# Kernel optimization log

Hardware: AMD Instinct MI355X
Metric: run time of the kernel (lower is better)

Reference implementation:

```python
import jax, jax.numpy as jnp
import numpy as np

D_IN, D_MODEL = 512, 256
B, N = 2, 512


def setup_inputs() -> dict:
    key = jax.random.key(0)
    ks = jax.random.split(key, 8)
    xav_x = float(np.sqrt(2.0 / (D_IN + D_MODEL)))
    xav_p = float(np.sqrt(2.0 / (4 + D_MODEL)))
    return {
        "x": jax.random.normal(ks[0], (B, N, D_IN), dtype=jnp.float32),
        "pos": jax.random.normal(ks[1], (B, N, 4), dtype=jnp.float32),
        "attn_mask": jax.random.randint(ks[2], (B, N, N), 0, 2, dtype=jnp.int32),
        "Wx": jax.random.normal(ks[3], (D_IN, D_MODEL), dtype=jnp.float32) * xav_x,
        "bx": jnp.zeros((D_MODEL,), dtype=jnp.float32),
        "Wp": jax.random.normal(ks[4], (4, D_MODEL), dtype=jnp.float32) * xav_p,
        "bp": jnp.zeros((D_MODEL,), dtype=jnp.float32),
        "w": jax.random.normal(ks[5], (D_MODEL,), dtype=jnp.float32) * 0.05,
    }


def reference(x, pos, attn_mask, Wx, bx, Wp, bp, w):
    # projected, activated inputs: [B, N, d_model]
    h = jnp.tanh(x @ Wx + bx)
    # pairwise relative positions: [B, N, N, 4]
    rel = pos[:, :, None, :] - pos[:, None, :, :]
    # position MLP + tanh: [B, N, N, d_model]
    z = jnp.tanh(rel @ Wp + bp)
    # scores via dot with weight vector: [B, N, N]
    attn = jnp.einsum("bijd,d->bij", z, w)
    mask = attn_mask != 0
    attn = jnp.where(mask, attn, -jnp.inf)
    attn = jax.nn.softmax(attn, axis=2)
    attn = jnp.where(mask, attn, 0.0)
    # dropout is identity in eval mode
    # weighted sum: [B, N, d_model]
    output = jnp.einsum("bij,bjd->bid", attn, h)
    return (output, attn)
```

## Files before the change

kernel.cpp:

```cpp
#include <hip/hip_runtime.h>
#include <hip/hip_bf16.h>
#include <math.h>

#define BATCH   2
#define SEQ     512
#define DIN     512
#define DM      256

#define LOG2E2  2.88539008177792681f

#if __has_builtin(__builtin_amdgcn_exp2f)
#define EXP2(x) __builtin_amdgcn_exp2f(x)
#else
#define EXP2(x) exp2f(x)
#endif
#if __has_builtin(__builtin_amdgcn_rcpf)
#define RCP(x) __builtin_amdgcn_rcpf(x)
#else
#define RCP(x) (1.0f / (x))
#endif

__device__ __forceinline__ float tanh_from_scaled(float targ) {
    return fmaf(-2.0f, RCP(1.0f + EXP2(targ)), 1.0f);
}

__global__ __launch_bounds__(512) void pre_k(
    const float* __restrict__ pos,
    const float* __restrict__ Wp,
    const float* __restrict__ bp,
    float* __restrict__ EA,
    float4* __restrict__ EB4)
{
    const int tid = threadIdx.x;

    if (blockIdx.x < 128) {
        const int b  = blockIdx.x >> 6;
        const int q  = blockIdx.x & 63;
        const int d0 = 4 * q;
        const float4 p = ((const float4*)pos)[b * SEQ + tid];
        float e[4];
        #pragma unroll
        for (int i = 0; i < 4; i++) {
            const int d = d0 + i;
            const float P = fmaf(p.x, Wp[d], fmaf(p.y, Wp[DM + d],
                            fmaf(p.z, Wp[2*DM + d], p.w * Wp[3*DM + d])));
            e[i] = EXP2(-LOG2E2 * P);
        }
        EB4[((size_t)(b * 64 + q)) * SEQ + tid] = make_float4(e[0], e[1], e[2], e[3]);
        return;
    }

    const int idx = blockIdx.x - 128;
    const int r2  = __builtin_amdgcn_readfirstlane(tid >> 8);
    const int d   = tid & 255;
    const int row = idx * 2 + r2;
    const float4 p = ((const float4*)pos)[row];
    const float P = fmaf(p.x, Wp[d],
                    fmaf(p.y, Wp[DM + d],
                    fmaf(p.z, Wp[2*DM + d],
                         p.w * Wp[3*DM + d])));
    EA[(size_t)row * DM + d] = EXP2(LOG2E2 * (P + bp[d]));
}

__global__ __launch_bounds__(256) void h_k(
    const float* __restrict__ x,
    const float* __restrict__ Wx,
    const float* __restrict__ bx,
    float* __restrict__ h)
{
    __shared__ float s_xt[32][68];
    __shared__ float s_wt[64][32];

    const int tid = threadIdx.x;
    const int rt  = blockIdx.x >> 3;
    const int ct  = blockIdx.x & 7;
    const int tx  = tid & 7;
    const int ty  = tid >> 3;

    float4 acc = make_float4(0.f, 0.f, 0.f, 0.f);

    for (int ks = 0; ks < 8; ks++) {
        const int k0 = ks * 64;
        #pragma unroll
        for (int s = 0; s < 2; s++) {
            const int fidx = tid * 2 + s;
            const int r = fidx >> 4, c = fidx & 15;
            const float4 v = *(const float4*)(x + (size_t)(rt * 32 + r) * DIN + k0 + 4 * c);
            *(float4*)&s_xt[r][4 * c] = v;
        }
        #pragma unroll
        for (int s = 0; s < 2; s++) {
            const int fidx = tid * 2 + s;
            const int r = fidx >> 3, c = fidx & 7;
            *(float4*)&s_wt[r][4 * c] =
                *(const float4*)(Wx + (size_t)(k0 + r) * DM + ct * 32 + 4 * c);
        }
        __syncthreads();

        #pragma unroll 8
        for (int k = 0; k < 64; k++) {
            const float  xv = s_xt[ty][k];
            const float4 wq = *(const float4*)&s_wt[k][4 * tx];
            acc.x = fmaf(xv, wq.x, acc.x);
            acc.y = fmaf(xv, wq.y, acc.y);
            acc.z = fmaf(xv, wq.z, acc.z);
            acc.w = fmaf(xv, wq.w, acc.w);
        }
        __syncthreads();
    }

    const float4 bq = *(const float4*)(bx + ct * 32 + 4 * tx);
    float4 t;
    t.x = tanh_from_scaled(LOG2E2 * (acc.x + bq.x));
    t.y = tanh_from_scaled(LOG2E2 * (acc.y + bq.y));
    t.z = tanh_from_scaled(LOG2E2 * (acc.z + bq.z));
    t.w = tanh_from_scaled(LOG2E2 * (acc.w + bq.w));
    *(float4*)(h + (size_t)(rt * 32 + ty) * DM + ct * 32 + 4 * tx) = t;
}

__global__ __launch_bounds__(512) void score_k(
    const int*   __restrict__ mask,
    const float* __restrict__ wv,
    const float* __restrict__ EA,
    const float4* __restrict__ EB4,
    float* __restrict__ attn_out)
{
    const int b   = blockIdx.x >> 8;
    const int i0  = (blockIdx.x & 255) * 2;
    const int tid = threadIdx.x;
    const int l   = tid & 63;

    __shared__ float4 s_eaA[64], s_eaB[64];
    __shared__ float  s_red[2][8];

    if (tid < 64) {
        s_eaA[tid] = *(const float4*)(EA + (size_t)(b * SEQ + i0) * DM + 4 * tid);
    } else if (tid < 128) {
        s_eaB[tid - 64] = *(const float4*)(EA + (size_t)(b * SEQ + i0 + 1) * DM + 4 * (tid - 64));
    }
    __syncthreads();

    const float4* __restrict__ EBj = EB4 + (size_t)b * 64 * SEQ + tid;

    float aA = 0.f, aB = 0.f;
    #pragma unroll 8
    for (int q = 0; q < 64; q++) {
        const float4 eb = EBj[(size_t)q * SEQ];
        const float4 eA = s_eaA[q];
        const float4 eB = s_eaB[q];
        const float4 wq = *(const float4*)(wv + 4 * q);

        const float yA0 = fmaf(eA.x, eb.x, 1.0f);
        const float yA1 = fmaf(eA.y, eb.y, 1.0f);
        const float yA2 = fmaf(eA.z, eb.z, 1.0f);
        const float yA3 = fmaf(eA.w, eb.w, 1.0f);
        aA = fmaf(fmaf(wq.y, yA0, wq.x * yA1), RCP(yA0 * yA1), aA);
        aA = fmaf(fmaf(wq.w, yA2, wq.z * yA3), RCP(yA2 * yA3), aA);

        const float yB0 = fmaf(eB.x, eb.x, 1.0f);
        const float yB1 = fmaf(eB.y, eb.y, 1.0f);
        const float yB2 = fmaf(eB.z, eb.z, 1.0f);
        const float yB3 = fmaf(eB.w, eb.w, 1.0f);
        aB = fmaf(fmaf(wq.y, yB0, wq.x * yB1), RCP(yB0 * yB1), aB);
        aB = fmaf(fmaf(wq.w, yB2, wq.z * yB3), RCP(yB2 * yB3), aB);
    }

    const size_t mrowA = (size_t)b * SEQ * SEQ + (size_t)i0 * SEQ + tid;
    const int mA = mask[mrowA];
    const int mB = mask[mrowA + SEQ];
    float pA = mA ? EXP2(-LOG2E2 * aA) : 0.f;
    float pB = mB ? EXP2(-LOG2E2 * aB) : 0.f;

    float sA = pA, sB = pB;
    #pragma unroll
    for (int off = 32; off; off >>= 1) {
        sA += __shfl_xor(sA, off, 64);
        sB += __shfl_xor(sB, off, 64);
    }
    const int w = tid >> 6;
    if (l == 0) { s_red[0][w] = sA; s_red[1][w] = sB; }
    __syncthreads();

    const float4 ra = ((const float4*)s_red[0])[0], rb = ((const float4*)s_red[0])[1];
    const float4 rc = ((const float4*)s_red[1])[0], rd = ((const float4*)s_red[1])[1];
    pA *= __fdividef(1.0f, (ra.x+ra.y+ra.z+ra.w) + (rb.x+rb.y+rb.z+rb.w));
    pB *= __fdividef(1.0f, (rc.x+rc.y+rc.z+rc.w) + (rd.x+rd.y+rd.z+rd.w));

    attn_out[mrowA]       = pA;
    attn_out[mrowA + SEQ] = pB;
}

__global__ __launch_bounds__(512) void av_k(
    const float* __restrict__ attn_out,
    const float* __restrict__ h,
    float* __restrict__ out)
{
    const int b   = blockIdx.x >> 7;
    const int i0  = (blockIdx.x & 127) * 4;
    const int tid = threadIdx.x;
    const int dq  = tid & 63;
    const int js  = __builtin_amdgcn_readfirstlane(tid >> 6);

    __shared__ float s_av[7][4][DM];

    const float* __restrict__ hp = h + (size_t)(b * SEQ + js * 64) * DM + 4 * dq;
    const float* __restrict__ ar0 = attn_out + (size_t)b * SEQ * SEQ
                                  + (size_t)i0 * SEQ + js * 64;
    const float* __restrict__ ar1 = ar0 + SEQ;
    const float* __restrict__ ar2 = ar0 + 2 * SEQ;
    const float* __restrict__ ar3 = ar0 + 3 * SEQ;

    float4 a0 = make_float4(0,0,0,0), a1 = a0, a2 = a0, a3 = a0;
    #pragma unroll 4
    for (int jj = 0; jj < 16; jj++) {
        const float4 P0 = *(const float4*)(ar0 + 4 * jj);
        const float4 P1 = *(const float4*)(ar1 + 4 * jj);
        const float4 P2 = *(const float4*)(ar2 + 4 * jj);
        const float4 P3 = *(const float4*)(ar3 + 4 * jj);
        const float4 h0 = *(const float4*)(hp + (size_t)(4*jj + 0) * DM);
        const float4 h1 = *(const float4*)(hp + (size_t)(4*jj + 1) * DM);
        const float4 h2 = *(const float4*)(hp + (size_t)(4*jj + 2) * DM);
        const float4 h3 = *(const float4*)(hp + (size_t)(4*jj + 3) * DM);

        a0.x = fmaf(P0.x,h0.x,fmaf(P0.y,h1.x,fmaf(P0.z,h2.x,fmaf(P0.w,h3.x,a0.x))));
        a0.y = fmaf(P0.x,h0.y,fmaf(P0.y,h1.y,fmaf(P0.z,h2.y,fmaf(P0.w,h3.y,a0.y))));
        a0.z = fmaf(P0.x,h0.z,fmaf(P0.y,h1.z,fmaf(P0.z,h2.z,fmaf(P0.w,h3.z,a0.z))));
        a0.w = fmaf(P0.x,h0.w,fmaf(P0.y,h1.w,fmaf(P0.z,h2.w,fmaf(P0.w,h3.w,a0.w))));
        a1.x = fmaf(P1.x,h0.x,fmaf(P1.y,h1.x,fmaf(P1.z,h2.x,fmaf(P1.w,h3.x,a1.x))));
        a1.y = fmaf(P1.x,h0.y,fmaf(P1.y,h1.y,fmaf(P1.z,h2.y,fmaf(P1.w,h3.y,a1.y))));
        a1.z = fmaf(P1.x,h0.z,fmaf(P1.y,h1.z,fmaf(P1.z,h2.z,fmaf(P1.w,h3.z,a1.z))));
        a1.w = fmaf(P1.x,h0.w,fmaf(P1.y,h1.w,fmaf(P1.z,h2.w,fmaf(P1.w,h3.w,a1.w))));
        a2.x = fmaf(P2.x,h0.x,fmaf(P2.y,h1.x,fmaf(P2.z,h2.x,fmaf(P2.w,h3.x,a2.x))));
        a2.y = fmaf(P2.x,h0.y,fmaf(P2.y,h1.y,fmaf(P2.z,h2.y,fmaf(P2.w,h3.y,a2.y))));
        a2.z = fmaf(P2.x,h0.z,fmaf(P2.y,h1.z,fmaf(P2.z,h2.z,fmaf(P2.w,h3.z,a2.z))));
        a2.w = fmaf(P2.x,h0.w,fmaf(P2.y,h1.w,fmaf(P2.z,h2.w,fmaf(P2.w,h3.w,a2.w))));
        a3.x = fmaf(P3.x,h0.x,fmaf(P3.y,h1.x,fmaf(P3.z,h2.x,fmaf(P3.w,h3.x,a3.x))));
        a3.y = fmaf(P3.x,h0.y,fmaf(P3.y,h1.y,fmaf(P3.z,h2.y,fmaf(P3.w,h3.y,a3.y))));
        a3.z = fmaf(P3.x,h0.z,fmaf(P3.y,h1.z,fmaf(P3.z,h2.z,fmaf(P3.w,h3.z,a3.z))));
        a3.w = fmaf(P3.x,h0.w,fmaf(P3.y,h1.w,fmaf(P3.z,h2.w,fmaf(P3.w,h3.w,a3.w))));
    }

    if (js > 0) {
        *(float4*)&s_av[js - 1][0][4 * dq] = a0;
        *(float4*)&s_av[js - 1][1][4 * dq] = a1;
        *(float4*)&s_av[js - 1][2][4 * dq] = a2;
        *(float4*)&s_av[js - 1][3][4 * dq] = a3;
    }
    __syncthreads();
    if (js == 0) {
        #pragma unroll
        for (int s = 0; s < 7; s++) {
            const float4 q0 = *(const float4*)&s_av[s][0][4 * dq];
            const float4 q1 = *(const float4*)&s_av[s][1][4 * dq];
            const float4 q2 = *(const float4*)&s_av[s][2][4 * dq];
            const float4 q3 = *(const float4*)&s_av[s][3][4 * dq];
            a0.x += q0.x; a0.y += q0.y; a0.z += q0.z; a0.w += q0.w;
            a1.x += q1.x; a1.y += q1.y; a1.z += q1.z; a1.w += q1.w;
            a2.x += q2.x; a2.y += q2.y; a2.z += q2.z; a2.w += q2.w;
            a3.x += q3.x; a3.y += q3.y; a3.z += q3.z; a3.w += q3.w;
        }
        float* __restrict__ op = out + (size_t)(b * SEQ + i0) * DM + 4 * dq;
        *(float4*)(op)          = a0;
        *(float4*)(op + DM)     = a1;
        *(float4*)(op + 2*DM)   = a2;
        *(float4*)(op + 3*DM)   = a3;
    }
}

extern "C" void kernel_launch(void* const* d_in, const int* in_sizes, int n_in,
                              void* d_out, int out_size, void* d_ws, size_t ws_size,
                              hipStream_t stream) {
    const float* x    = (const float*)d_in[0];
    const float* pos  = (const float*)d_in[1];
    const int*   mask = (const int*)  d_in[2];
    const float* Wx   = (const float*)d_in[3];
    const float* bx   = (const float*)d_in[4];
    const float* Wp   = (const float*)d_in[5];
    const float* bp   = (const float*)d_in[6];
    const float* wv   = (const float*)d_in[7];

    float* out      = (float*)d_out;
    float* attn_out = (float*)d_out + (size_t)BATCH*SEQ*DM;

    char*   ws  = (char*)d_ws;
    float*  h   = (float*)(ws);
    float*  EA  = (float*)(ws + (size_t)BATCH*SEQ*DM*4);
    float4* EB4 = (float4*)(ws + 2*(size_t)BATCH*SEQ*DM*4);

    pre_k  <<<128 + (BATCH*SEQ)/2, 512, 0, stream>>>(pos, Wp, bp, EA, EB4);
    h_k    <<<256, 256, 0, stream>>>(x, Wx, bx, h);
    score_k<<<(BATCH*SEQ)/2, 512, 0, stream>>>(mask, wv, EA, EB4, attn_out);
    av_k   <<<(BATCH*SEQ)/4, 512, 0, stream>>>(attn_out, h, out);
}
```

Measured before the change: 114.5 us.

## Fuse four kernels into two: merge producers and fuse score with AV

Merges the EA/EB precompute and the x@Wx+tanh projection into one producer kernel, and fuses the softmax-score kernel with the attention-times-h reduction so probabilities stay in shared memory instead of being re-read from global. The number of launches drops from four to two. The h projection now reads Wx directly from global memory instead of staging it in LDS, and each attend block redoes the h reads for only two rows instead of four, which raises total h traffic.

```diff
diff --git a/kernel.cpp b/kernel.cpp
--- a/kernel.cpp
+++ b/kernel.cpp
@@ -24,12 +24,16 @@
     return fmaf(-2.0f, RCP(1.0f + EXP2(targ)), 1.0f);
 }
 
-__global__ __launch_bounds__(512) void pre_k(
+__global__ __launch_bounds__(512) void produce_k(
     const float* __restrict__ pos,
     const float* __restrict__ Wp,
     const float* __restrict__ bp,
+    const float* __restrict__ x,
+    const float* __restrict__ Wx,
+    const float* __restrict__ bx,
     float* __restrict__ EA,
-    float4* __restrict__ EB4)
+    float4* __restrict__ EB4,
+    float* __restrict__ h)
 {
     const int tid = threadIdx.x;
 
@@ -50,57 +54,44 @@
         return;
     }
 
-    const int idx = blockIdx.x - 128;
-    const int r2  = __builtin_amdgcn_readfirstlane(tid >> 8);
-    const int d   = tid & 255;
-    const int row = idx * 2 + r2;
-    const float4 p = ((const float4*)pos)[row];
-    const float P = fmaf(p.x, Wp[d],
-                    fmaf(p.y, Wp[DM + d],
-                    fmaf(p.z, Wp[2*DM + d],
-                         p.w * Wp[3*DM + d])));
-    EA[(size_t)row * DM + d] = EXP2(LOG2E2 * (P + bp[d]));
-}
-
-__global__ __launch_bounds__(256) void h_k(
-    const float* __restrict__ x,
-    const float* __restrict__ Wx,
-    const float* __restrict__ bx,
-    float* __restrict__ h)
-{
     __shared__ float s_xt[32][68];
-    __shared__ float s_wt[64][32];
-
-    const int tid = threadIdx.x;
-    const int rt  = blockIdx.x >> 3;
-    const int ct  = blockIdx.x & 7;
-    const int tx  = tid & 7;
-    const int ty  = tid >> 3;
+
+    const int idx  = blockIdx.x - 128;
+    const int rt   = idx >> 2;
+    const int ct   = idx & 3;
+    const int ty   = tid >> 4;
+    const int tx   = tid & 15;
+    const int row  = rt * 32 + ty;
+    const int dcol = ct * 64 + 4 * tx;
+
+    {
+        const float4 p  = ((const float4*)pos)[row];
+        const float4 w0 = *(const float4*)(Wp + dcol);
+        const float4 w1 = *(const float4*)(Wp + DM + dcol);
+        const float4 w2 = *(const float4*)(Wp + 2*DM + dcol);
+        const float4 w3 = *(const float4*)(Wp + 3*DM + dcol);
+        const float4 bq = *(const float4*)(bp + dcol);
+        float4 ea;
+        ea.x = EXP2(LOG2E2 * (fmaf(p.x,w0.x,fmaf(p.y,w1.x,fmaf(p.z,w2.x,p.w*w3.x))) + bq.x));
+        ea.y = EXP2(LOG2E2 * (fmaf(p.x,w0.y,fmaf(p.y,w1.y,fmaf(p.z,w2.y,p.w*w3.y))) + bq.y));
+        ea.z = EXP2(LOG2E2 * (fmaf(p.x,w0.z,fmaf(p.y,w1.z,fmaf(p.z,w2.z,p.w*w3.z))) + bq.z));
+        ea.w = EXP2(LOG2E2 * (fmaf(p.x,w0.w,fmaf(p.y,w1.w,fmaf(p.z,w2.w,p.w*w3.w))) + bq.w));
+        *(float4*)(EA + (size_t)row * DM + dcol) = ea;
+    }
 
     float4 acc = make_float4(0.f, 0.f, 0.f, 0.f);
 
     for (int ks = 0; ks < 8; ks++) {
         const int k0 = ks * 64;
-        #pragma unroll
-        for (int s = 0; s < 2; s++) {
-            const int fidx = tid * 2 + s;
-            const int r = fidx >> 4, c = fidx & 15;
-            const float4 v = *(const float4*)(x + (size_t)(rt * 32 + r) * DIN + k0 + 4 * c);
-            *(float4*)&s_xt[r][4 * c] = v;
-        }
-        #pragma unroll
-        for (int s = 0; s < 2; s++) {
-            const int fidx = tid * 2 + s;
-            const int r = fidx >> 3, c = fidx & 7;
-            *(float4*)&s_wt[r][4 * c] =
-                *(const float4*)(Wx + (size_t)(k0 + r) * DM + ct * 32 + 4 * c);
-        }
+        *(float4*)&s_xt[ty][4 * tx] =
+            *(const float4*)(x + (size_t)row * DIN + k0 + 4 * tx);
         __syncthreads();
 
+        const float* __restrict__ wxk = Wx + (size_t)k0 * DM + dcol;
         #pragma unroll 8
         for (int k = 0; k < 64; k++) {
             const float  xv = s_xt[ty][k];
-            const float4 wq = *(const float4*)&s_wt[k][4 * tx];
+            const float4 wq = *(const float4*)(wxk + (size_t)k * DM);
             acc.x = fmaf(xv, wq.x, acc.x);
             acc.y = fmaf(xv, wq.y, acc.y);
             acc.z = fmaf(xv, wq.z, acc.z);
@@ -109,20 +100,22 @@
         __syncthreads();
     }
 
-    const float4 bq = *(const float4*)(bx + ct * 32 + 4 * tx);
+    const float4 bq4 = *(const float4*)(bx + dcol);
     float4 t;
-    t.x = tanh_from_scaled(LOG2E2 * (acc.x + bq.x));
-    t.y = tanh_from_scaled(LOG2E2 * (acc.y + bq.y));
-    t.z = tanh_from_scaled(LOG2E2 * (acc.z + bq.z));
-    t.w = tanh_from_scaled(LOG2E2 * (acc.w + bq.w));
-    *(float4*)(h + (size_t)(rt * 32 + ty) * DM + ct * 32 + 4 * tx) = t;
-}
-
-__global__ __launch_bounds__(512) void score_k(
+    t.x = tanh_from_scaled(LOG2E2 * (acc.x + bq4.x));
+    t.y = tanh_from_scaled(LOG2E2 * (acc.y + bq4.y));
+    t.z = tanh_from_scaled(LOG2E2 * (acc.z + bq4.z));
+    t.w = tanh_from_scaled(LOG2E2 * (acc.w + bq4.w));
+    *(float4*)(h + (size_t)row * DM + dcol) = t;
+}
+
+__global__ __launch_bounds__(512) void attend_k(
     const int*   __restrict__ mask,
     const float* __restrict__ wv,
     const float* __restrict__ EA,
     const float4* __restrict__ EB4,
+    const float* __restrict__ h,
+    float* __restrict__ out,
     float* __restrict__ attn_out)
 {
     const int b   = blockIdx.x >> 8;
@@ -131,7 +124,9 @@
     const int l   = tid & 63;
 
     __shared__ float4 s_eaA[64], s_eaB[64];
+    __shared__ float  s_p[2][SEQ];
     __shared__ float  s_red[2][8];
+    __shared__ float  s_o[7][2][DM];
 
     if (tid < 64) {
         s_eaA[tid] = *(const float4*)(EA + (size_t)(b * SEQ + i0) * DM + 4 * tid);
@@ -177,8 +172,7 @@
         sA += __shfl_xor(sA, off, 64);
         sB += __shfl_xor(sB, off, 64);
     }
-    const int w = tid >> 6;
-    if (l == 0) { s_red[0][w] = sA; s_red[1][w] = sB; }
+    if (l == 0) { s_red[0][tid >> 6] = sA; s_red[1][tid >> 6] = sB; }
     __syncthreads();
 
     const float4 ra = ((const float4*)s_red[0])[0], rb = ((const float4*)s_red[0])[1];
@@ -188,35 +182,21 @@
 
     attn_out[mrowA]       = pA;
     attn_out[mrowA + SEQ] = pB;
-}
-
-__global__ __launch_bounds__(512) void av_k(
-    const float* __restrict__ attn_out,
-    const float* __restrict__ h,
-    float* __restrict__ out)
-{
-    const int b   = blockIdx.x >> 7;
-    const int i0  = (blockIdx.x & 127) * 4;
-    const int tid = threadIdx.x;
-    const int dq  = tid & 63;
-    const int js  = __builtin_amdgcn_readfirstlane(tid >> 6);
-
-    __shared__ float s_av[7][4][DM];
-
+    s_p[0][tid] = pA;
+    s_p[1][tid] = pB;
+    __syncthreads();
+
+    const int dq = tid & 63;
+    const int js = __builtin_amdgcn_readfirstlane(tid >> 6);
     const float* __restrict__ hp = h + (size_t)(b * SEQ + js * 64) * DM + 4 * dq;
-    const float* __restrict__ ar0 = attn_out + (size_t)b * SEQ * SEQ
-                                  + (size_t)i0 * SEQ + js * 64;
-    const float* __restrict__ ar1 = ar0 + SEQ;
-    const float* __restrict__ ar2 = ar0 + 2 * SEQ;
-    const float* __restrict__ ar3 = ar0 + 3 * SEQ;
-
-    float4 a0 = make_float4(0,0,0,0), a1 = a0, a2 = a0, a3 = a0;
+    const float* __restrict__ p0 = &s_p[0][js * 64];
+    const float* __restrict__ p1 = &s_p[1][js * 64];
+
+    float4 a0 = make_float4(0,0,0,0), a1 = a0;
     #pragma unroll 4
     for (int jj = 0; jj < 16; jj++) {
-        const float4 P0 = *(const float4*)(ar0 + 4 * jj);
-        const float4 P1 = *(const float4*)(ar1 + 4 * jj);
-        const float4 P2 = *(const float4*)(ar2 + 4 * jj);
-        const float4 P3 = *(const float4*)(ar3 + 4 * jj);
+        const float4 P0 = *(const float4*)(p0 + 4 * jj);
+        const float4 P1 = *(const float4*)(p1 + 4 * jj);
         const float4 h0 = *(const float4*)(hp + (size_t)(4*jj + 0) * DM);
         const float4 h1 = *(const float4*)(hp + (size_t)(4*jj + 1) * DM);
         const float4 h2 = *(const float4*)(hp + (size_t)(4*jj + 2) * DM);
@@ -230,40 +210,24 @@
         a1.y = fmaf(P1.x,h0.y,fmaf(P1.y,h1.y,fmaf(P1.z,h2.y,fmaf(P1.w,h3.y,a1.y))));
         a1.z = fmaf(P1.x,h0.z,fmaf(P1.y,h1.z,fmaf(P1.z,h2.z,fmaf(P1.w,h3.z,a1.z))));
         a1.w = fmaf(P1.x,h0.w,fmaf(P1.y,h1.w,fmaf(P1.z,h2.w,fmaf(P1.w,h3.w,a1.w))));
-        a2.x = fmaf(P2.x,h0.x,fmaf(P2.y,h1.x,fmaf(P2.z,h2.x,fmaf(P2.w,h3.x,a2.x))));
-        a2.y = fmaf(P2.x,h0.y,fmaf(P2.y,h1.y,fmaf(P2.z,h2.y,fmaf(P2.w,h3.y,a2.y))));
-        a2.z = fmaf(P2.x,h0.z,fmaf(P2.y,h1.z,fmaf(P2.z,h2.z,fmaf(P2.w,h3.z,a2.z))));
-        a2.w = fmaf(P2.x,h0.w,fmaf(P2.y,h1.w,fmaf(P2.z,h2.w,fmaf(P2.w,h3.w,a2.w))));
-        a3.x = fmaf(P3.x,h0.x,fmaf(P3.y,h1.x,fmaf(P3.z,h2.x,fmaf(P3.w,h3.x,a3.x))));
-        a3.y = fmaf(P3.x,h0.y,fmaf(P3.y,h1.y,fmaf(P3.z,h2.y,fmaf(P3.w,h3.y,a3.y))));
-        a3.z = fmaf(P3.x,h0.z,fmaf(P3.y,h1.z,fmaf(P3.z,h2.z,fmaf(P3.w,h3.z,a3.z))));
-        a3.w = fmaf(P3.x,h0.w,fmaf(P3.y,h1.w,fmaf(P3.z,h2.w,fmaf(P3.w,h3.w,a3.w))));
     }
 
     if (js > 0) {
-        *(float4*)&s_av[js - 1][0][4 * dq] = a0;
-        *(float4*)&s_av[js - 1][1][4 * dq] = a1;
-        *(float4*)&s_av[js - 1][2][4 * dq] = a2;
-        *(float4*)&s_av[js - 1][3][4 * dq] = a3;
+        *(float4*)&s_o[js - 1][0][4 * dq] = a0;
+        *(float4*)&s_o[js - 1][1][4 * dq] = a1;
     }
     __syncthreads();
     if (js == 0) {
         #pragma unroll
         for (int s = 0; s < 7; s++) {
-            const float4 q0 = *(const float4*)&s_av[s][0][4 * dq];
-            const float4 q1 = *(const float4*)&s_av[s][1][4 * dq];
-            const float4 q2 = *(const float4*)&s_av[s][2][4 * dq];
-            const float4 q3 = *(const float4*)&s_av[s][3][4 * dq];
+            const float4 q0 = *(const float4*)&s_o[s][0][4 * dq];
+            const float4 q1 = *(const float4*)&s_o[s][1][4 * dq];
             a0.x += q0.x; a0.y += q0.y; a0.z += q0.z; a0.w += q0.w;
             a1.x += q1.x; a1.y += q1.y; a1.z += q1.z; a1.w += q1.w;
-            a2.x += q2.x; a2.y += q2.y; a2.z += q2.z; a2.w += q2.w;
-            a3.x += q3.x; a3.y += q3.y; a3.z += q3.z; a3.w += q3.w;
         }
         float* __restrict__ op = out + (size_t)(b * SEQ + i0) * DM + 4 * dq;
-        *(float4*)(op)          = a0;
-        *(float4*)(op + DM)     = a1;
-        *(float4*)(op + 2*DM)   = a2;
-        *(float4*)(op + 3*DM)   = a3;
+        *(float4*)(op)      = a0;
+        *(float4*)(op + DM) = a1;
     }
 }
 
@@ -287,8 +251,6 @@
     float*  EA  = (float*)(ws + (size_t)BATCH*SEQ*DM*4);
     float4* EB4 = (float4*)(ws + 2*(size_t)BATCH*SEQ*DM*4);
 
-    pre_k  <<<128 + (BATCH*SEQ)/2, 512, 0, stream>>>(pos, Wp, bp, EA, EB4);
-    h_k    <<<256, 256, 0, stream>>>(x, Wx, bx, h);
-    score_k<<<(BATCH*SEQ)/2, 512, 0, stream>>>(mask, wv, EA, EB4, attn_out);
-    av_k   <<<(BATCH*SEQ)/4, 512, 0, stream>>>(attn_out, h, out);
-}
+    produce_k<<<256, 512, 0, stream>>>(pos, Wp, bp, x, Wx, bx, EA, EB4, h);
+    attend_k <<<(BATCH*SEQ)/2, 512, 0, stream>>>(mask, wv, EA, EB4, h, out, attn_out);
+}
```

Result: slower. 133.8 us (+16.9%).

## Fuse score softmax and attention-value product into one kernel

Applied to the files above, without the earlier changes.

Merges the score/softmax kernel with the attn@h kernel so each block keeps its two rows of normalized probabilities in shared memory and immediately computes the weighted sum over h. This removes one kernel launch and the re-read of the attention matrix from global memory. In exchange each block now handles 2 rows instead of 4 in the AV stage, so h is re-read twice as often overall, and shared memory use per block grows.

```diff
diff --git a/kernel.cpp b/kernel.cpp
--- a/kernel.cpp
+++ b/kernel.cpp
@@ -118,11 +118,13 @@
     *(float4*)(h + (size_t)(rt * 32 + ty) * DM + ct * 32 + 4 * tx) = t;
 }
 
-__global__ __launch_bounds__(512) void score_k(
+__global__ __launch_bounds__(512) void attend_k(
     const int*   __restrict__ mask,
     const float* __restrict__ wv,
     const float* __restrict__ EA,
     const float4* __restrict__ EB4,
+    const float* __restrict__ h,
+    float* __restrict__ out,
     float* __restrict__ attn_out)
 {
     const int b   = blockIdx.x >> 8;
@@ -131,7 +133,9 @@
     const int l   = tid & 63;
 
     __shared__ float4 s_eaA[64], s_eaB[64];
+    __shared__ float  s_p[2][SEQ];
     __shared__ float  s_red[2][8];
+    __shared__ float  s_o[7][2][DM];
 
     if (tid < 64) {
         s_eaA[tid] = *(const float4*)(EA + (size_t)(b * SEQ + i0) * DM + 4 * tid);
@@ -177,8 +181,7 @@
         sA += __shfl_xor(sA, off, 64);
         sB += __shfl_xor(sB, off, 64);
     }
-    const int w = tid >> 6;
-    if (l == 0) { s_red[0][w] = sA; s_red[1][w] = sB; }
+    if (l == 0) { s_red[0][tid >> 6] = sA; s_red[1][tid >> 6] = sB; }
     __syncthreads();
 
     const float4 ra = ((const float4*)s_red[0])[0], rb = ((const float4*)s_red[0])[1];
@@ -188,35 +191,21 @@
 
     attn_out[mrowA]       = pA;
     attn_out[mrowA + SEQ] = pB;
-}
-
-__global__ __launch_bounds__(512) void av_k(
-    const float* __restrict__ attn_out,
-    const float* __restrict__ h,
-    float* __restrict__ out)
-{
-    const int b   = blockIdx.x >> 7;
-    const int i0  = (blockIdx.x & 127) * 4;
-    const int tid = threadIdx.x;
-    const int dq  = tid & 63;
-    const int js  = __builtin_amdgcn_readfirstlane(tid >> 6);
-
-    __shared__ float s_av[7][4][DM];
-
+    s_p[0][tid] = pA;
+    s_p[1][tid] = pB;
+    __syncthreads();
+
+    const int dq = tid & 63;
+    const int js = __builtin_amdgcn_readfirstlane(tid >> 6);
     const float* __restrict__ hp = h + (size_t)(b * SEQ + js * 64) * DM + 4 * dq;
-    const float* __restrict__ ar0 = attn_out + (size_t)b * SEQ * SEQ
-                                  + (size_t)i0 * SEQ + js * 64;
-    const float* __restrict__ ar1 = ar0 + SEQ;
-    const float* __restrict__ ar2 = ar0 + 2 * SEQ;
-    const float* __restrict__ ar3 = ar0 + 3 * SEQ;
-
-    float4 a0 = make_float4(0,0,0,0), a1 = a0, a2 = a0, a3 = a0;
+    const float* __restrict__ p0 = &s_p[0][js * 64];
+    const float* __restrict__ p1 = &s_p[1][js * 64];
+
+    float4 a0 = make_float4(0,0,0,0), a1 = a0;
     #pragma unroll 4
     for (int jj = 0; jj < 16; jj++) {
-        const float4 P0 = *(const float4*)(ar0 + 4 * jj);
-        const float4 P1 = *(const float4*)(ar1 + 4 * jj);
-        const float4 P2 = *(const float4*)(ar2 + 4 * jj);
-        const float4 P3 = *(const float4*)(ar3 + 4 * jj);
+        const float4 P0 = *(const float4*)(p0 + 4 * jj);
+        const float4 P1 = *(const float4*)(p1 + 4 * jj);
         const float4 h0 = *(const float4*)(hp + (size_t)(4*jj + 0) * DM);
         const float4 h1 = *(const float4*)(hp + (size_t)(4*jj + 1) * DM);
         const float4 h2 = *(const float4*)(hp + (size_t)(4*jj + 2) * DM);
@@ -230,40 +219,24 @@
         a1.y = fmaf(P1.x,h0.y,fmaf(P1.y,h1.y,fmaf(P1.z,h2.y,fmaf(P1.w,h3.y,a1.y))));
         a1.z = fmaf(P1.x,h0.z,fmaf(P1.y,h1.z,fmaf(P1.z,h2.z,fmaf(P1.w,h3.z,a1.z))));
         a1.w = fmaf(P1.x,h0.w,fmaf(P1.y,h1.w,fmaf(P1.z,h2.w,fmaf(P1.w,h3.w,a1.w))));
-        a2.x = fmaf(P2.x,h0.x,fmaf(P2.y,h1.x,fmaf(P2.z,h2.x,fmaf(P2.w,h3.x,a2.x))));
-        a2.y = fmaf(P2.x,h0.y,fmaf(P2.y,h1.y,fmaf(P2.z,h2.y,fmaf(P2.w,h3.y,a2.y))));
-        a2.z = fmaf(P2.x,h0.z,fmaf(P2.y,h1.z,fmaf(P2.z,h2.z,fmaf(P2.w,h3.z,a2.z))));
-        a2.w = fmaf(P2.x,h0.w,fmaf(P2.y,h1.w,fmaf(P2.z,h2.w,fmaf(P2.w,h3.w,a2.w))));
-        a3.x = fmaf(P3.x,h0.x,fmaf(P3.y,h1.x,fmaf(P3.z,h2.x,fmaf(P3.w,h3.x,a3.x))));
-        a3.y = fmaf(P3.x,h0.y,fmaf(P3.y,h1.y,fmaf(P3.z,h2.y,fmaf(P3.w,h3.y,a3.y))));
-        a3.z = fmaf(P3.x,h0.z,fmaf(P3.y,h1.z,fmaf(P3.z,h2.z,fmaf(P3.w,h3.z,a3.z))));
-        a3.w = fmaf(P3.x,h0.w,fmaf(P3.y,h1.w,fmaf(P3.z,h2.w,fmaf(P3.w,h3.w,a3.w))));
     }
 
     if (js > 0) {
-        *(float4*)&s_av[js - 1][0][4 * dq] = a0;
-        *(float4*)&s_av[js - 1][1][4 * dq] = a1;
-        *(float4*)&s_av[js - 1][2][4 * dq] = a2;
-        *(float4*)&s_av[js - 1][3][4 * dq] = a3;
+        *(float4*)&s_o[js - 1][0][4 * dq] = a0;
+        *(float4*)&s_o[js - 1][1][4 * dq] = a1;
     }
     __syncthreads();
     if (js == 0) {
         #pragma unroll
         for (int s = 0; s < 7; s++) {
-            const float4 q0 = *(const float4*)&s_av[s][0][4 * dq];
-            const float4 q1 = *(const float4*)&s_av[s][1][4 * dq];
-            const float4 q2 = *(const float4*)&s_av[s][2][4 * dq];
-            const float4 q3 = *(const float4*)&s_av[s][3][4 * dq];
+            const float4 q0 = *(const float4*)&s_o[s][0][4 * dq];
+            const float4 q1 = *(const float4*)&s_o[s][1][4 * dq];
             a0.x += q0.x; a0.y += q0.y; a0.z += q0.z; a0.w += q0.w;
             a1.x += q1.x; a1.y += q1.y; a1.z += q1.z; a1.w += q1.w;
-            a2.x += q2.x; a2.y += q2.y; a2.z += q2.z; a2.w += q2.w;
-            a3.x += q3.x; a3.y += q3.y; a3.z += q3.z; a3.w += q3.w;
         }
         float* __restrict__ op = out + (size_t)(b * SEQ + i0) * DM + 4 * dq;
-        *(float4*)(op)          = a0;
-        *(float4*)(op + DM)     = a1;
-        *(float4*)(op + 2*DM)   = a2;
-        *(float4*)(op + 3*DM)   = a3;
+        *(float4*)(op)      = a0;
+        *(float4*)(op + DM) = a1;
     }
 }
 
@@ -287,8 +260,7 @@
     float*  EA  = (float*)(ws + (size_t)BATCH*SEQ*DM*4);
     float4* EB4 = (float4*)(ws + 2*(size_t)BATCH*SEQ*DM*4);
 
-    pre_k  <<<128 + (BATCH*SEQ)/2, 512, 0, stream>>>(pos, Wp, bp, EA, EB4);
-    h_k    <<<256, 256, 0, stream>>>(x, Wx, bx, h);
-    score_k<<<(BATCH*SEQ)/2, 512, 0, stream>>>(mask, wv, EA, EB4, attn_out);
-    av_k   <<<(BATCH*SEQ)/4, 512, 0, stream>>>(attn_out, h, out);
-}
+    pre_k   <<<128 + (BATCH*SEQ)/2, 512, 0, stream>>>(pos, Wp, bp, EA, EB4);
+    h_k     <<<256, 256, 0, stream>>>(x, Wx, bx, h);
+    attend_k<<<(BATCH*SEQ)/2, 512, 0, stream>>>(mask, wv, EA, EB4, h, out, attn_out);
+}
```

Measured after the change: 114.4 us. No clear change (-0.0%).
